# Kernel optimization log

Hardware: AMD Instinct MI355X
Metric: run time of the kernel (lower is better)

The kernel has to match this reference:

```python
import jax, jax.numpy as jnp
import numpy as np

K = 7  # median blur kernel size

def median_blur(x, k=K):
    # kornia.filters.median_blur: zero padding, gather kxk window per pixel,
    # torch.median -> lower median = sorted index (k*k-1)//2 (== k*k//2 for odd k*k)
    pad = k // 2
    B, C, H, W = x.shape
    xp = jnp.pad(x, ((0, 0), (0, 0), (pad, pad), (pad, pad)))
    # [B, C, k*k, H, W] patch tensor (same as kornia's unfold via binary-kernel conv)
    patches = jnp.stack(
        [xp[:, :, i:i + H, j:j + W] for i in range(k) for j in range(k)], axis=2
    )
    return jnp.sort(patches, axis=2)[:, :, (k * k) // 2]


def setup_inputs() -> dict:
    key = jax.random.key(0)
    k1, k2 = jax.random.split(key)
    image = jax.random.normal(k1, (16, 3, 256, 256), dtype=jnp.float32)
    cover_image = jax.random.normal(k2, (16, 3, 256, 256), dtype=jnp.float32)
    return {"image": image, "cover_image": cover_image}


def reference(image, cover_image):
    x = (image + 1.0) / 2.0          # [-1,1] -> [0,1]
    x = median_blur(x, K)            # 7x7 median filter (p=1.0, always applied)
    x = x * 2.0 - 1.0                # [0,1] -> [-1,1]
    return jnp.clip(x, -1.0, 1.0)
```

## Files before the change

kernel.cpp:

```cpp
#include <hip/hip_runtime.h>
#include <stdint.h>


#define IMG_H 256
#define IMG_W 256
#define RROWS 8
#define RUNS  (IMG_H / RROWS)

#define PERM(a,b,s) __builtin_amdgcn_perm((a),(b),(s))

struct Planes { uint32_t pL[7], pH[7]; };

__device__ __forceinline__ Planes transpose7(
    uint32_t L0, uint32_t L1, uint32_t L2, uint32_t L3, uint32_t L4, uint32_t L5, uint32_t L6,
    uint32_t H0, uint32_t H1, uint32_t H2, uint32_t H3, uint32_t H4, uint32_t H5, uint32_t H6)
{
    Planes P;
    {
        uint32_t za1 = PERM(L1, L0, 0x05010400u), zb1 = PERM(L1, L0, 0x07030602u);
        uint32_t za2 = PERM(L3, L2, 0x05010400u), zb2 = PERM(L3, L2, 0x07030602u);
        uint32_t za3 = PERM(L5, L4, 0x05010400u), zb3 = PERM(L5, L4, 0x07030602u);
        uint32_t za4 = PERM(0u, L6, 0x05010400u), zb4 = PERM(0u, L6, 0x07030602u);
        P.pL[0] = PERM(za2, za1, 0x05040100u);  P.pH[0] = PERM(za4, za3, 0x05040100u);
        P.pL[1] = PERM(za2, za1, 0x07060302u);  P.pH[1] = PERM(za4, za3, 0x07060302u);
        P.pL[2] = PERM(zb2, zb1, 0x05040100u);  P.pH[2] = PERM(zb4, zb3, 0x05040100u);
        P.pL[3] = PERM(zb2, zb1, 0x07060302u);  P.pH[3] = PERM(zb4, zb3, 0x07060302u);
    }
    {
        uint32_t za1 = PERM(H1, H0, 0x05010400u), zb1 = PERM(H1, H0, 0x07030602u);
        uint32_t za2 = PERM(H3, H2, 0x05010400u), zb2 = PERM(H3, H2, 0x07030602u);
        uint32_t za3 = PERM(H5, H4, 0x05010400u), zb3 = PERM(H5, H4, 0x07030602u);
        uint32_t za4 = PERM(0u, H6, 0x05010400u), zb4 = PERM(0u, H6, 0x07030602u);
        P.pL[4] = PERM(za2, za1, 0x05040100u);  P.pH[4] = PERM(za4, za3, 0x05040100u);
        P.pL[5] = PERM(za2, za1, 0x07060302u);  P.pH[5] = PERM(za4, za3, 0x07060302u);
        P.pL[6] = PERM(zb2, zb1, 0x05040100u);  P.pH[6] = PERM(zb4, zb3, 0x05040100u);
    }
    return P;
}

__global__ __launch_bounds__(256, 6)
void median7_kernel(const float* __restrict__ img, float* __restrict__ out) {
    const int x     = threadIdx.x;
    const int plane = blockIdx.x / RUNS;
    const int run   = blockIdx.x % RUNS;
    const int y0    = run * RROWS;

    const float* ip = img + (size_t)plane * (IMG_H * IMG_W);
    float*       op = out + (size_t)plane * (IMG_H * IMG_W);

    __shared__ ulonglong2 VL[2][IMG_W + 6];
    if (x < 3) {
        const ulonglong2 z = make_ulonglong2(0ULL, 0ULL);
        VL[0][x] = z; VL[1][x] = z;
        VL[0][IMG_W + 3 + x] = z; VL[1][IMG_W + 3 + x] = z;
    }

    uint32_t vlo = 0u, vhi = 0u;

    auto loadrow = [&](int ry) -> float {
        int rc = min(max(ry, 0), IMG_H - 1);
        return ip[rc * IMG_W + x];
    };
    auto insert_v = [&](float v, int ry) {
        float t = fmaf(v, 63.5f, 64.0f);
        t = fminf(fmaxf(t, 0.0f), 127.0f);
        uint32_t q = (uint32_t)t;
        q = ((uint32_t)ry < (uint32_t)IMG_H) ? q : 0u;
        uint32_t nlo = ((q & 15u) * 0x08102040u) & 0x40404040u;
        uint32_t nhi = ((q >> 4)  * 0x08102040u) & 0x40404040u;
        vlo = ((vlo >> 1) & 0x3F3F3F3Fu) | nlo;
        vhi = ((vhi >> 1) & 0x3F3F3F3Fu) | nhi;
    };

#pragma unroll
    for (int j = 0; j < 6; ++j) insert_v(loadrow(y0 - 3 + j), y0 - 3 + j);
    insert_v(loadrow(y0 + 3), y0 + 3);
    uint32_t palo = vlo, pahi = vhi;
    insert_v(loadrow(y0 + 4), y0 + 4);
    uint32_t pblo = vlo, pbhi = vhi;
    VL[0][3 + x] = make_ulonglong2(((unsigned long long)pahi << 32) | palo,
                                   ((unsigned long long)pbhi << 32) | pblo);
    float f0 = loadrow(y0 + 5), f1 = loadrow(y0 + 6);
    __syncthreads();

#pragma unroll
    for (int i = 0; i < RROWS / 2; ++i) {
        const int buf = i & 1;

        const ulonglong2* qp = &VL[buf][x];
        ulonglong2 n0 = qp[0], n1 = qp[1], n2 = qp[2];
        ulonglong2 n4 = qp[4], n5 = qp[5], n6 = qp[6];

        const uint32_t calo = palo, cahi = pahi, cblo = pblo, cbhi = pbhi;

        if (i < 3) {
            insert_v(f0, y0 + 5 + 2 * i);
            palo = vlo; pahi = vhi;
            insert_v(f1, y0 + 6 + 2 * i);
            pblo = vlo; pbhi = vhi;
            VL[buf ^ 1][3 + x] =
                make_ulonglong2(((unsigned long long)pahi << 32) | palo,
                                ((unsigned long long)pbhi << 32) | pblo);
        }
        if (i < 2) { f0 = loadrow(y0 + 7 + 2 * i); f1 = loadrow(y0 + 8 + 2 * i); }

        Planes PA = transpose7(
            (uint32_t)n0.x, (uint32_t)n1.x, (uint32_t)n2.x, calo,
            (uint32_t)n4.x, (uint32_t)n5.x, (uint32_t)n6.x,
            (uint32_t)(n0.x >> 32), (uint32_t)(n1.x >> 32), (uint32_t)(n2.x >> 32), cahi,
            (uint32_t)(n4.x >> 32), (uint32_t)(n5.x >> 32), (uint32_t)(n6.x >> 32));
        Planes PB = transpose7(
            (uint32_t)n0.y, (uint32_t)n1.y, (uint32_t)n2.y, cblo,
            (uint32_t)n4.y, (uint32_t)n5.y, (uint32_t)n6.y,
            (uint32_t)(n0.y >> 32), (uint32_t)(n1.y >> 32), (uint32_t)(n2.y >> 32), cbhi,
            (uint32_t)(n4.y >> 32), (uint32_t)(n5.y >> 32), (uint32_t)(n6.y >> 32));

        uint32_t acloA = 0x7F7F7F7Fu, achiA = 0x007F7F7Fu, kA = 25u, medA = 0u;
        uint32_t acloB = 0x7F7F7F7Fu, achiB = 0x007F7F7Fu, kB = 25u, medB = 0u;
#pragma unroll
        for (int p = 6; p >= 0; --p) {
            {
                uint32_t ol = acloA & PA.pL[p], oh = achiA & PA.pH[p];
                uint32_t c1 = (uint32_t)(__popc(ol) + __popc(oh));
                bool b = (kA <= c1);
                acloA = b ? ol : (acloA ^ ol);
                achiA = b ? oh : (achiA ^ oh);
                kA    = b ? kA : (kA - c1);
                medA  = (medA << 1) | (b ? 1u : 0u);
            }
            {
                uint32_t ol = acloB & PB.pL[p], oh = achiB & PB.pH[p];
                uint32_t c1 = (uint32_t)(__popc(ol) + __popc(oh));
                bool b = (kB <= c1);
                acloB = b ? ol : (acloB ^ ol);
                achiB = b ? oh : (achiB ^ oh);
                kB    = b ? kB : (kB - c1);
                medB  = (medB << 1) | (b ? 1u : 0u);
            }
        }

        __builtin_nontemporal_store(fmaf((float)medA, 2.0f / 127.0f, -1.0f),
                                    &op[(y0 + 2 * i) * IMG_W + x]);
        __builtin_nontemporal_store(fmaf((float)medB, 2.0f / 127.0f, -1.0f),
                                    &op[(y0 + 2 * i + 1) * IMG_W + x]);

        __syncthreads();
    }
}

extern "C" void kernel_launch(void* const* d_in, const int* in_sizes, int n_in,
                              void* d_out, int out_size, void* d_ws, size_t ws_size,
                              hipStream_t stream) {
    const float* img = (const float*)d_in[0];
    float* out = (float*)d_out;
    const int planes = in_sizes[0] / (IMG_H * IMG_W);
    dim3 grid(planes * RUNS);
    dim3 block(256);
    median7_kernel<<<grid, block, 0, stream>>>(img, out);
}
```

Measured before the change: 17.77 us.

## Give each wavefront a private LDS strip with halo to drop block barriers

Each 64-lane wavefront now owns its own LDS strip of 70 entries. Six lanes additionally load and roll the halo columns, so neighbour column bit-planes never cross wavefront boundaries. This removes all __syncthreads barriers and the double buffer, relying on compiler memory fences and lockstep wavefront execution instead. The cost is redundant halo global loads and quantisation work, and correctness depends on wave-synchronous LDS visibility without an explicit barrier.

After: 20.52 us. 15.5% more time.

```diff
diff --git a/kernel.cpp b/kernel.cpp
--- a/kernel.cpp
+++ b/kernel.cpp
@@ -8,6 +8,7 @@
 #define RUNS  (IMG_H / RROWS)
 
 #define PERM(a,b,s) __builtin_amdgcn_perm((a),(b),(s))
+#define MEMFENCE()  asm volatile("" ::: "memory")
 
 struct Planes { uint32_t pL[7], pH[7]; };
 
@@ -38,71 +39,95 @@
     return P;
 }
 
+__device__ __forceinline__ uint32_t quant7(float v) {
+    float t = fmaf(v, 63.5f, 64.0f);
+    t = fminf(fmaxf(t, 0.0f), 127.0f);
+    return (uint32_t)t;
+}
+__device__ __forceinline__ void roll(uint32_t& lo, uint32_t& hi, uint32_t q) {
+    uint32_t nlo = ((q & 15u) * 0x08102040u) & 0x40404040u;
+    uint32_t nhi = ((q >> 4)  * 0x08102040u) & 0x40404040u;
+    lo = ((lo >> 1) & 0x3F3F3F3Fu) | nlo;
+    hi = ((hi >> 1) & 0x3F3F3F3Fu) | nhi;
+}
+
 __global__ __launch_bounds__(256, 6)
 void median7_kernel(const float* __restrict__ img, float* __restrict__ out) {
-    const int x     = threadIdx.x;
-    const int plane = blockIdx.x / RUNS;
-    const int run   = blockIdx.x % RUNS;
-    const int y0    = run * RROWS;
-
-    const float* ip = img + (size_t)plane * (IMG_H * IMG_W);
-    float*       op = out + (size_t)plane * (IMG_H * IMG_W);
-
-    __shared__ ulonglong2 VL[2][IMG_W + 6];
-    if (x < 3) {
-        const ulonglong2 z = make_ulonglong2(0ULL, 0ULL);
-        VL[0][x] = z; VL[1][x] = z;
-        VL[0][IMG_W + 3 + x] = z; VL[1][IMG_W + 3 + x] = z;
-    }
+    const int lane = threadIdx.x & 63;
+    const int wv   = threadIdx.x >> 6;
+    const int pl   = blockIdx.x / RUNS;
+    const int run  = blockIdx.x % RUNS;
+    const int y0   = run * RROWS;
+    const int W    = wv * 64;
+    const int xo   = W + lane;
+
+    const float* ip = img + (size_t)pl * (IMG_H * IMG_W);
+    float*       op = out + (size_t)pl * (IMG_H * IMG_W);
+
+    __shared__ ulonglong2 VL[4][70];
+    ulonglong2* strip = VL[wv];
+
+    const bool hl    = (lane < 6);
+    const int  hx    = W + ((lane < 3) ? (lane - 3) : (61 + lane));
+    const int  hslot = (lane < 3) ? lane : (64 + lane);
+    const bool hok   = hl && ((uint32_t)hx < (uint32_t)IMG_W);
+    const int  hxc   = min(max(hx, 0), IMG_W - 1);
 
     uint32_t vlo = 0u, vhi = 0u;
-
-    auto loadrow = [&](int ry) -> float {
-        int rc = min(max(ry, 0), IMG_H - 1);
-        return ip[rc * IMG_W + x];
-    };
-    auto insert_v = [&](float v, int ry) {
-        float t = fmaf(v, 63.5f, 64.0f);
-        t = fminf(fmaxf(t, 0.0f), 127.0f);
-        uint32_t q = (uint32_t)t;
-        q = ((uint32_t)ry < (uint32_t)IMG_H) ? q : 0u;
-        uint32_t nlo = ((q & 15u) * 0x08102040u) & 0x40404040u;
-        uint32_t nhi = ((q >> 4)  * 0x08102040u) & 0x40404040u;
-        vlo = ((vlo >> 1) & 0x3F3F3F3Fu) | nlo;
-        vhi = ((vhi >> 1) & 0x3F3F3F3Fu) | nhi;
-    };
-
-#pragma unroll
-    for (int j = 0; j < 6; ++j) insert_v(loadrow(y0 - 3 + j), y0 - 3 + j);
-    insert_v(loadrow(y0 + 3), y0 + 3);
-    uint32_t palo = vlo, pahi = vhi;
-    insert_v(loadrow(y0 + 4), y0 + 4);
-    uint32_t pblo = vlo, pbhi = vhi;
-    VL[0][3 + x] = make_ulonglong2(((unsigned long long)pahi << 32) | palo,
-                                   ((unsigned long long)pbhi << 32) | pblo);
-    float f0 = loadrow(y0 + 5), f1 = loadrow(y0 + 6);
-    __syncthreads();
+    uint32_t wlo = 0u, whi = 0u;
+
+    {
+        float pv[6], ph[6];
+#pragma unroll
+        for (int j = 0; j < 6; ++j) {
+            int rc = max(y0 - 3 + j, 0);
+            pv[j] = ip[rc * IMG_W + xo];
+            ph[j] = hl ? ip[rc * IMG_W + hxc] : 0.0f;
+        }
+#pragma unroll
+        for (int j = 0; j < 6; ++j) {
+            bool rok = (y0 - 3 + j) >= 0;
+            roll(vlo, vhi, rok ? quant7(pv[j]) : 0u);
+            roll(wlo, whi, (rok && hok) ? quant7(ph[j]) : 0u);
+        }
+    }
+
+    uint32_t palo, pahi, pblo, pbhi;
+    {
+        float f0 = ip[(y0 + 3) * IMG_W + xo], f1 = ip[(y0 + 4) * IMG_W + xo];
+        float g0 = hl ? ip[(y0 + 3) * IMG_W + hxc] : 0.0f;
+        float g1 = hl ? ip[(y0 + 4) * IMG_W + hxc] : 0.0f;
+        roll(vlo, vhi, quant7(f0)); palo = vlo; pahi = vhi;
+        roll(vlo, vhi, quant7(f1)); pblo = vlo; pbhi = vhi;
+        strip[3 + lane] = make_ulonglong2(
+            ((unsigned long long)pahi << 32) | palo,
+            ((unsigned long long)pbhi << 32) | pblo);
+        roll(wlo, whi, hok ? quant7(g0) : 0u);
+        uint32_t halo1 = wlo, hahi1 = whi;
+        roll(wlo, whi, hok ? quant7(g1) : 0u);
+        if (hl)
+            strip[hslot] = make_ulonglong2(
+                ((unsigned long long)hahi1 << 32) | halo1,
+                ((unsigned long long)whi << 32) | wlo);
+    }
+    MEMFENCE();
+    ulonglong2 n0 = strip[lane],     n1 = strip[lane + 1], n2 = strip[lane + 2];
+    ulonglong2 n4 = strip[lane + 4], n5 = strip[lane + 5], n6 = strip[lane + 6];
 
 #pragma unroll
     for (int i = 0; i < RROWS / 2; ++i) {
-        const int buf = i & 1;
-
-        const ulonglong2* qp = &VL[buf][x];
-        ulonglong2 n0 = qp[0], n1 = qp[1], n2 = qp[2];
-        ulonglong2 n4 = qp[4], n5 = qp[5], n6 = qp[6];
-
         const uint32_t calo = palo, cahi = pahi, cblo = pblo, cbhi = pbhi;
 
+        float f0 = 0.0f, f1 = 0.0f, g0 = 0.0f, g1 = 0.0f;
+        bool r0ok = true, r1ok = true;
         if (i < 3) {
-            insert_v(f0, y0 + 5 + 2 * i);
-            palo = vlo; pahi = vhi;
-            insert_v(f1, y0 + 6 + 2 * i);
-            pblo = vlo; pbhi = vhi;
-            VL[buf ^ 1][3 + x] =
-                make_ulonglong2(((unsigned long long)pahi << 32) | palo,
-                                ((unsigned long long)pbhi << 32) | pblo);
-        }
-        if (i < 2) { f0 = loadrow(y0 + 7 + 2 * i); f1 = loadrow(y0 + 8 + 2 * i); }
+            int ry0 = y0 + 5 + 2 * i, ry1 = ry0 + 1;
+            r0ok = ry0 < IMG_H; r1ok = ry1 < IMG_H;
+            int rc0 = min(ry0, IMG_H - 1), rc1 = min(ry1, IMG_H - 1);
+            f0 = ip[rc0 * IMG_W + xo];
+            f1 = ip[rc1 * IMG_W + xo];
+            if (hl) { g0 = ip[rc0 * IMG_W + hxc]; g1 = ip[rc1 * IMG_W + hxc]; }
+        }
 
         Planes PA = transpose7(
             (uint32_t)n0.x, (uint32_t)n1.x, (uint32_t)n2.x, calo,
@@ -140,11 +165,28 @@
         }
 
         __builtin_nontemporal_store(fmaf((float)medA, 2.0f / 127.0f, -1.0f),
-                                    &op[(y0 + 2 * i) * IMG_W + x]);
+                                    &op[(y0 + 2 * i) * IMG_W + xo]);
         __builtin_nontemporal_store(fmaf((float)medB, 2.0f / 127.0f, -1.0f),
-                                    &op[(y0 + 2 * i + 1) * IMG_W + x]);
-
-        __syncthreads();
+                                    &op[(y0 + 2 * i + 1) * IMG_W + xo]);
+
+        if (i < 3) {
+            MEMFENCE();
+            roll(vlo, vhi, r0ok ? quant7(f0) : 0u); palo = vlo; pahi = vhi;
+            roll(vlo, vhi, r1ok ? quant7(f1) : 0u); pblo = vlo; pbhi = vhi;
+            strip[3 + lane] = make_ulonglong2(
+                ((unsigned long long)pahi << 32) | palo,
+                ((unsigned long long)pbhi << 32) | pblo);
+            roll(wlo, whi, (r0ok && hok) ? quant7(g0) : 0u);
+            uint32_t halo1 = wlo, hahi1 = whi;
+            roll(wlo, whi, (r1ok && hok) ? quant7(g1) : 0u);
+            if (hl)
+                strip[hslot] = make_ulonglong2(
+                    ((unsigned long long)hahi1 << 32) | halo1,
+                    ((unsigned long long)whi << 32) | wlo);
+            MEMFENCE();
+            n0 = strip[lane];     n1 = strip[lane + 1]; n2 = strip[lane + 2];
+            n4 = strip[lane + 4]; n5 = strip[lane + 5]; n6 = strip[lane + 6];
+        }
     }
 }
 
```
